# Kernel optimization log

Hardware: AMD Instinct MI355X
Metric: run time of the kernel (lower is better)

Reference implementation:

```python
import jax, jax.numpy as jnp
import numpy as np

N, E, B = 50000, 100000, 512   # nodes, edges, graphs
H, F_NODE, F_EDGE, T_OUT = 64, 16, 8, 1
T = 3                           # message-passing steps


def setup_inputs() -> dict:
    key = jax.random.key(0)
    ks = jax.random.split(key, 18)

    def w(k, shape, fan_in):
        return jax.random.normal(k, shape, dtype=jnp.float32) / np.sqrt(fan_in)

    return {
        "node_features": jax.random.normal(ks[0], (N, F_NODE), dtype=jnp.float32),
        "edge_features": jax.random.normal(ks[1], (E, F_EDGE), dtype=jnp.float32),
        "Esrc": jax.random.randint(ks[2], (E,), 0, N, dtype=jnp.int32),
        "Etgt": jax.random.randint(ks[3], (E,), 0, N, dtype=jnp.int32),
        "batch": jnp.sort(jax.random.randint(ks[4], (N,), 0, B, dtype=jnp.int32)),
        # input linear: node_features -> hidden
        "Win": w(ks[5], (H, F_NODE), F_NODE),
        "bin_": jnp.zeros((H,), jnp.float32),
        # edge encoder MLP: edge_features -> hidden -> hidden*hidden
        "We1": w(ks[6], (H, F_EDGE), F_EDGE),
        "be1": jnp.zeros((H,), jnp.float32),
        "We2": w(ks[7], (H * H, H), H),
        "be2": jnp.zeros((H * H,), jnp.float32),
        # GRU cell (shared across T steps)
        "Wih": w(ks[8], (3 * H, H), H),
        "bih": jnp.zeros((3 * H,), jnp.float32),
        "Whh": w(ks[9], (3 * H, H), H),
        "bhh": jnp.zeros((3 * H,), jnp.float32),
        # output linear: hidden -> target_features
        "Wout": w(ks[10], (T_OUT, H), H),
        "bout": jnp.zeros((T_OUT,), jnp.float32),
    }


def _gru(x, h, Wih, bih, Whh, bhh):
    gi = x @ Wih.T + bih            # [N, 3H]
    gh = h @ Whh.T + bhh
    i_r, i_z, i_n = jnp.split(gi, 3, axis=-1)
    h_r, h_z, h_n = jnp.split(gh, 3, axis=-1)
    r = jax.nn.sigmoid(i_r + h_r)
    z = jax.nn.sigmoid(i_z + h_z)
    n = jnp.tanh(i_n + r * h_n)
    return (1.0 - z) * n + z * h


def reference(node_features, edge_features, Esrc, Etgt, batch,
              Win, bin_, We1, be1, We2, be2,
              Wih, bih, Whh, bhh, Wout, bout):
    # Edge encoder MLP -> per-edge [H, H] message matrix (ENN style)
    eh = jax.nn.relu(edge_features @ We1.T + be1)          # [E, H]
    edge_data = (eh @ We2.T + be2).reshape(E, H, H)        # [E, H, H]

    x = node_features @ Win.T + bin_                       # [N, H]

    for _ in range(T):  # small fixed layer count
        msg = jnp.einsum('eij,ej->ei', edge_data, x[Esrc])  # per-edge matvec
        agg = jax.ops.segment_sum(msg, Etgt, num_segments=N)
        x = _gru(agg, x, Wih, bih, Whh, bhh)

    out = x @ Wout.T + bout                                # [N, 1]
    pooled = jax.ops.segment_sum(out, batch, num_segments=B)  # [B, 1]
    return pooled
```

## Files before the change

### kernel.cpp

```cpp
#include <hip/hip_runtime.h>
#include <hip/hip_fp16.h>

#define NN 50000
#define NE 100000
#define NB 512

typedef _Float16 f16x8 __attribute__((ext_vector_type(8)));
typedef _Float16 f16x4 __attribute__((ext_vector_type(4)));
typedef float f32x4  __attribute__((ext_vector_type(4)));
typedef float f32x16 __attribute__((ext_vector_type(16)));

__device__ __forceinline__ float sigm(float v) { return 1.0f / (1.0f + __expf(-v)); }
__device__ __forceinline__ float tanh_fast(float v) {
    float e = __expf(-2.0f * fabsf(v));
    float t = (1.0f - e) / (1.0f + e);
    return v < 0.f ? -t : t;
}

__global__ void fill0_kernel(float4* __restrict__ p, int n4)
{
    int i = blockIdx.x * 256 + threadIdx.x;
    const int stride = gridDim.x * 256;
    for (; i < n4; i += stride) p[i] = make_float4(0.f, 0.f, 0.f, 0.f);
}

__global__ __launch_bounds__(256) void node_in_kernel(
    const float* __restrict__ nf, const float* __restrict__ Win,
    const float* __restrict__ bin_, float* __restrict__ x, __half* __restrict__ xh)
{
    int idx = blockIdx.x * 256 + threadIdx.x;
    if (idx >= NN * 64) return;
    int n = idx >> 6, h = idx & 63;
    float acc = bin_[h];
    #pragma unroll
    for (int f = 0; f < 16; f++) acc += nf[n * 16 + f] * Win[h * 16 + f];
    x[idx] = acc;
    xh[idx] = __float2half(acc);
}

__global__ __launch_bounds__(256) void edge_l1_kernel(
    const float* __restrict__ ef, const float* __restrict__ We1,
    const float* __restrict__ be1, __half* __restrict__ ehh)
{
    int idx = blockIdx.x * 256 + threadIdx.x;
    if (idx >= NE * 64) return;
    int e = idx >> 6, k = idx & 63;
    float acc = be1[k];
    #pragma unroll
    for (int f = 0; f < 8; f++) acc += ef[e * 8 + f] * We1[k * 8 + f];
    ehh[idx] = __float2half(fmaxf(acc, 0.0f));
}

__global__ __launch_bounds__(256) void pack_b32_kernel(
    const float* __restrict__ We2, const float* __restrict__ be2,
    __half* __restrict__ Bp)
{
    int idx = blockIdx.x * 256 + threadIdx.x;
    if (idx >= 260 * 1024) return;
    int i  = idx & 7;
    int n  = (idx >> 3) & 31;
    int hi = (idx >> 8) & 1;
    int nt = (idx >> 9) & 1;
    int kt = idx >> 10;
    int p  = kt * 16 + hi * 8 + i;
    int col = nt * 32 + n;
    float v;
    if (p < 4096) {
        int j = p >> 6, k = p & 63;
        v = We2[((size_t)(col * 64 + j)) * 64 + k];
    } else {
        v = be2[col * 64 + (p - 4096)];
    }
    Bp[idx] = __float2half(v);
}

__global__ __launch_bounds__(256) void pack_gru_kernel(
    const float* __restrict__ Wih, const float* __restrict__ Whh,
    __half* __restrict__ WG)
{
    int idx = blockIdx.x * 256 + threadIdx.x;
    if (idx >= 24576) return;
    int kk = idx & 31;
    int n  = (idx >> 5) & 15;
    int nt = (idx >> 9) % 24;
    int kt = (idx >> 9) / 24;
    int k = kt * 32 + kk;
    int col192 = (nt % 12) * 16 + n;
    int gate = col192 >> 6, h = col192 & 63;
    const float* src = (nt < 12) ? Wih : Whh;
    WG[idx] = __float2half(src[((size_t)(gate * 64 + h)) * 64 + k]);
}

__global__ __launch_bounds__(128) void msg_kernel(
    const __half* __restrict__ xh, const __half* __restrict__ ehh,
    const __half* __restrict__ Bp,
    const int* __restrict__ Esrc, const int* __restrict__ Etgt,
    float* __restrict__ agg)
{
    __shared__ __attribute__((aligned(16))) __half xs[256 * 72];
    __shared__ __attribute__((aligned(16))) __half bst[16 * 1024];
    __shared__ int tgt_s[256];
    const int tid = threadIdx.x;
    const int e0 = blockIdx.x * 256;
    const int w = tid >> 6, lane = tid & 63;
    const int n32 = lane & 31, hi = lane >> 5;

    #pragma unroll
    for (int rr = 0; rr < 2; rr++) {
        const int row = rr * 128 + tid;
        const int e = e0 + row;
        const bool ok = (e < NE);
        const int src = ok ? Esrc[e] : 0;
        tgt_s[row] = ok ? Etgt[e] : -1;
        const uint4* xsrc = (const uint4*)(xh + (size_t)src * 64);
        #pragma unroll
        for (int i = 0; i < 8; i++) {
            uint4 v = ok ? xsrc[i] : make_uint4(0, 0, 0, 0);
            *(uint4*)(&xs[row * 72 + i * 8]) = v;
        }
    }

    __half2 ehc[4][4][4];
    #pragma unroll
    for (int mt = 0; mt < 4; mt++) {
        const int e = e0 + w * 128 + mt * 32 + n32;
        if (e < NE) {
            #pragma unroll
            for (int c4 = 0; c4 < 4; c4++) {
                union { uint4 u; __half2 h[4]; } u;
                u.u = *(const uint4*)(ehh + (size_t)e * 64 + c4 * 16 + hi * 8);
                #pragma unroll
                for (int q = 0; q < 4; q++) ehc[mt][c4][q] = u.h[q];
            }
        } else {
            __half2 z = __half2half2(__float2half(0.f));
            #pragma unroll
            for (int c4 = 0; c4 < 4; c4++)
                #pragma unroll
                for (int q = 0; q < 4; q++) ehc[mt][c4][q] = z;
        }
    }

    f32x16 acc[4][2];
    #pragma unroll
    for (int a = 0; a < 4; a++)
        #pragma unroll
        for (int b = 0; b < 2; b++)
            #pragma unroll
            for (int q = 0; q < 16; q++) acc[a][b][q] = 0.f;

    const __half* blane = bst + hi * 256 + n32 * 8;
    const int rbase = w * 128;

    #pragma unroll 1
    for (int c = 0; c < 17; c++) {
        const int niter = (c < 16) ? 16 : 4;
        __syncthreads();
        {
            const __half* gsrc = Bp + (size_t)c * 16384;
            for (int i = 0; i < niter; i++)
                *(uint4*)(bst + (size_t)(i * 128 + tid) * 8) =
                    *(const uint4*)(gsrc + (size_t)(i * 128 + tid) * 8);
        }
        __syncthreads();

        if (c < 16) {
            f16x4 xr4[4];
            #pragma unroll
            for (int mt = 0; mt < 4; mt++)
                xr4[mt] = *(const f16x4*)(xs + (rbase + mt * 32 + n32) * 72 + c * 4);
            #pragma unroll
            for (int u = 0; u < 16; u++) {
                f16x8 b0 = *(const f16x8*)(blane + u * 1024);
                f16x8 b1 = *(const f16x8*)(blane + u * 1024 + 512);
                const int c4 = u & 3;
                const int jq = u >> 2;
                #pragma unroll
                for (int mt = 0; mt < 4; mt++) {
                    union { f16x4 v; __half h[4]; } xu; xu.v = xr4[mt];
                    __half2 xv2 = __half2half2(xu.h[jq]);
                    union { __half2 h[4]; f16x8 v; } a;
                    #pragma unroll
                    for (int q = 0; q < 4; q++) a.h[q] = __hmul2(xv2, ehc[mt][c4][q]);
                    acc[mt][0] = __builtin_amdgcn_mfma_f32_32x32x16_f16(a.v, b0, acc[mt][0], 0, 0, 0);
                    acc[mt][1] = __builtin_amdgcn_mfma_f32_32x32x16_f16(a.v, b1, acc[mt][1], 0, 0, 0);
                }
            }
        } else {
            #pragma unroll
            for (int u = 0; u < 4; u++) {
                f16x8 b0 = *(const f16x8*)(blane + u * 1024);
                f16x8 b1 = *(const f16x8*)(blane + u * 1024 + 512);
                #pragma unroll
                for (int mt = 0; mt < 4; mt++) {
                    f16x8 a = *(const f16x8*)(xs + (rbase + mt * 32 + n32) * 72 + u * 16 + hi * 8);
                    acc[mt][0] = __builtin_amdgcn_mfma_f32_32x32x16_f16(a, b0, acc[mt][0], 0, 0, 0);
                    acc[mt][1] = __builtin_amdgcn_mfma_f32_32x32x16_f16(a, b1, acc[mt][1], 0, 0, 0);
                }
            }
        }
    }

    #pragma unroll
    for (int mt = 0; mt < 4; mt++) {
        #pragma unroll
        for (int r = 0; r < 16; r++) {
            const int rowe = (r & 3) + 8 * (r >> 2) + 4 * hi;
            const int t = tgt_s[rbase + mt * 32 + rowe];
            if (t >= 0) {
                atomicAdd(agg + (size_t)t * 64 + n32, acc[mt][0][r]);
                atomicAdd(agg + (size_t)t * 64 + 32 + n32, acc[mt][1][r]);
            }
        }
    }
}

__global__ __launch_bounds__(256, 2) void gru_kernel(
    const float* __restrict__ agg, float* __restrict__ x, __half* __restrict__ xh,
    const __half* __restrict__ WG,
    const float* __restrict__ bih, const float* __restrict__ bhh)
{
    __shared__ __attribute__((aligned(16))) __half wlds[24576];
    __shared__ __attribute__((aligned(16))) __half aggh[64 * 72];
    __shared__ __attribute__((aligned(16))) float xbuf[64 * 68];
    const int tid = threadIdx.x;
    const int node0 = blockIdx.x * 64;

    {
        const uint4* src = (const uint4*)WG;
        uint4* dst = (uint4*)wlds;
        #pragma unroll
        for (int i = 0; i < 12; i++) dst[i * 256 + tid] = src[i * 256 + tid];
    }
    #pragma unroll
    for (int i = 0; i < 4; i++) {
        int idx4 = i * 256 + tid;
        int nl = idx4 >> 4, c4 = idx4 & 15;
        int node = node0 + nl;
        float4 a = make_float4(0.f, 0.f, 0.f, 0.f);
        float4 xv = make_float4(0.f, 0.f, 0.f, 0.f);
        if (node < NN) {
            a  = *(const float4*)(agg + (size_t)node * 64 + c4 * 4);
            xv = *(const float4*)(x   + (size_t)node * 64 + c4 * 4);
        }
        __half2* ah = (__half2*)(aggh + nl * 72 + c4 * 4);
        ah[0] = __floats2half2_rn(a.x, a.y);
        ah[1] = __floats2half2_rn(a.z, a.w);
        *(float4*)(xbuf + nl * 68 + c4 * 4) = xv;
    }
    __syncthreads();

    const int w = tid >> 6, lane = tid & 63, m = lane & 15, quad = lane >> 4;
    const int nl_a = w * 16 + m;

    f16x8 a_agg[2], a_x[2];
    #pragma unroll
    for (int kt = 0; kt < 2; kt++) {
        const int koff = kt * 32 + quad * 8;
        a_agg[kt] = *(const f16x8*)(aggh + nl_a * 72 + koff);
        const float* xp = xbuf + nl_a * 68 + koff;
        union { __half2 h[4]; f16x8 v; } u;
        u.h[0] = __floats2half2_rn(xp[0], xp[1]);
        u.h[1] = __floats2half2_rn(xp[2], xp[3]);
        u.h[2] = __floats2half2_rn(xp[4], xp[5]);
        u.h[3] = __floats2half2_rn(xp[6], xp[7]);
        a_x[kt] = u.v;
    }

    f32x4 acc[24];
    #pragma unroll
    for (int nt = 0; nt < 24; nt++)
        #pragma unroll
        for (int q = 0; q < 4; q++) acc[nt][q] = 0.f;

    #pragma unroll
    for (int kt = 0; kt < 2; kt++) {
        #pragma unroll
        for (int nt = 0; nt < 24; nt++) {
            f16x8 b = *(const f16x8*)(wlds + (kt * 24 + nt) * 512 + m * 32 + quad * 8);
            acc[nt] = __builtin_amdgcn_mfma_f32_16x16x32_f16(
                (nt < 12) ? a_agg[kt] : a_x[kt], b, acc[nt], 0, 0, 0);
        }
    }

    #pragma unroll
    for (int t = 0; t < 4; t++) {
        const int h = t * 16 + m;
        const float bir = bih[h], biz = bih[64 + h], bin = bih[128 + h];
        const float bhr = bhh[h], bhz = bhh[64 + h], bhn = bhh[128 + h];
        #pragma unroll
        for (int r = 0; r < 4; r++) {
            const int nl = w * 16 + quad * 4 + r;
            float ir  = acc[t][r]      + bir;
            float iz  = acc[4 + t][r]  + biz;
            float in_ = acc[8 + t][r]  + bin;
            float hr  = acc[12 + t][r] + bhr;
            float hz  = acc[16 + t][r] + bhz;
            float hn  = acc[20 + t][r] + bhn;
            float rg = sigm(ir + hr);
            float z  = sigm(iz + hz);
            float n  = tanh_fast(in_ + rg * hn);
            float xold = xbuf[nl * 68 + h];
            xbuf[nl * 68 + h] = (1.0f - z) * n + z * xold;
        }
    }
    __syncthreads();

    #pragma unroll
    for (int i = 0; i < 4; i++) {
        int idx4 = i * 256 + tid;
        int nl = idx4 >> 4, c4 = idx4 & 15;
        int node = node0 + nl;
        if (node < NN) {
            float4 v = *(const float4*)(xbuf + nl * 68 + c4 * 4);
            *(float4*)(x + (size_t)node * 64 + c4 * 4) = v;
        }
    }
    #pragma unroll
    for (int i = 0; i < 2; i++) {
        int idx8 = i * 256 + tid;
        int nl = idx8 >> 3, c8 = idx8 & 7;
        int node = node0 + nl;
        if (node < NN) {
            const float* xp = xbuf + nl * 68 + c8 * 8;
            union { __half2 h[4]; uint4 u; } u;
            u.h[0] = __floats2half2_rn(xp[0], xp[1]);
            u.h[1] = __floats2half2_rn(xp[2], xp[3]);
            u.h[2] = __floats2half2_rn(xp[4], xp[5]);
            u.h[3] = __floats2half2_rn(xp[6], xp[7]);
            *(uint4*)(xh + (size_t)node * 64 + c8 * 8) = u.u;
        }
    }
}

__global__ __launch_bounds__(256) void pool_kernel(
    const float* __restrict__ x, const float* __restrict__ Wout,
    const float* __restrict__ bout, const int* __restrict__ batch,
    float* __restrict__ out)
{
    const int node = blockIdx.x * 256 + threadIdx.x;
    if (node >= NN) return;
    float acc = bout[0];
    const float4* xp = (const float4*)(x + (size_t)node * 64);
    #pragma unroll
    for (int i = 0; i < 16; i++) {
        float4 v = xp[i];
        acc += v.x * Wout[4*i] + v.y * Wout[4*i+1] + v.z * Wout[4*i+2] + v.w * Wout[4*i+3];
    }
    atomicAdd(out + batch[node], acc);
}

extern "C" void kernel_launch(void* const* d_in, const int* in_sizes, int n_in,
                              void* d_out, int out_size, void* d_ws, size_t ws_size,
                              hipStream_t stream)
{
    const float* nf   = (const float*)d_in[0];
    const float* ef   = (const float*)d_in[1];
    const int*   Esrc = (const int*)  d_in[2];
    const int*   Etgt = (const int*)  d_in[3];
    const int*   bat  = (const int*)  d_in[4];
    const float* Win  = (const float*)d_in[5];
    const float* bin_ = (const float*)d_in[6];
    const float* We1  = (const float*)d_in[7];
    const float* be1  = (const float*)d_in[8];
    const float* We2  = (const float*)d_in[9];
    const float* be2  = (const float*)d_in[10];
    const float* Wih  = (const float*)d_in[11];
    const float* bih  = (const float*)d_in[12];
    const float* Whh  = (const float*)d_in[13];
    const float* bhh  = (const float*)d_in[14];
    const float* Wout = (const float*)d_in[15];
    const float* bout = (const float*)d_in[16];

    char* ws = (char*)d_ws;
    float*  x   = (float*)(ws);
    float*  agg = (float*)(ws + 12800000);
    __half* xh  = (__half*)(ws + 25600000);
    __half* ehh = (__half*)(ws + 32000000);
    __half* Bp  = (__half*)(ws + 44800000);
    __half* WG  = (__half*)(ws + 45400064);

    hipMemsetAsync(d_out, 0, NB * sizeof(float), stream);

    node_in_kernel<<<(NN * 64 + 255) / 256, 256, 0, stream>>>(nf, Win, bin_, x, xh);
    edge_l1_kernel<<<(NE * 64 + 255) / 256, 256, 0, stream>>>(ef, We1, be1, ehh);
    pack_b32_kernel<<<(260 * 1024 + 255) / 256, 256, 0, stream>>>(We2, be2, Bp);
    pack_gru_kernel<<<(24576 + 255) / 256, 256, 0, stream>>>(Wih, Whh, WG);

    for (int t = 0; t < 3; t++) {
        fill0_kernel<<<1024, 256, 0, stream>>>((float4*)agg, NN * 16);
        msg_kernel<<<(NE + 255) / 256, 128, 0, stream>>>(xh, ehh, Bp, Esrc, Etgt, agg);
        gru_kernel<<<(NN + 63) / 64, 256, 0, stream>>>(agg, x, xh, WG, bih, bhh);
    }

    pool_kernel<<<(NN + 255) / 256, 256, 0, stream>>>(x, Wout, bout, bat, (float*)d_out);
}
```

Measured before the change: 486.7 us.

## Split msg kernel over K halves, drop fp32 state, fuse final GRU with pooling

The message kernel now launches two blocks per 256-edge tile, each covering half of the j-range, and reads B fragments straight from global/L2 instead of staging them through LDS with per-chunk barriers. The fp32 node state is removed, so the GRU reads and writes only the fp16 copy. The GRU kernel now zeroes agg itself, replacing the separate fill kernels. The last GRU step is fused with the output projection and per-graph pooling. This cuts launches, memory traffic and LDS synchronisation, but doubles the atomic adds into agg and keeps the hidden state in fp16 between steps, which may reduce accuracy.

```diff
diff --git a/kernel.cpp b/kernel.cpp
--- a/kernel.cpp
+++ b/kernel.cpp
@@ -26,7 +26,7 @@
 
 __global__ __launch_bounds__(256) void node_in_kernel(
     const float* __restrict__ nf, const float* __restrict__ Win,
-    const float* __restrict__ bin_, float* __restrict__ x, __half* __restrict__ xh)
+    const float* __restrict__ bin_, __half* __restrict__ xh)
 {
     int idx = blockIdx.x * 256 + threadIdx.x;
     if (idx >= NN * 64) return;
@@ -34,7 +34,6 @@
     float acc = bin_[h];
     #pragma unroll
     for (int f = 0; f < 16; f++) acc += nf[n * 16 + f] * Win[h * 16 + f];
-    x[idx] = acc;
     xh[idx] = __float2half(acc);
 }
 
@@ -91,17 +90,17 @@
     WG[idx] = __float2half(src[((size_t)(gate * 64 + h)) * 64 + k]);
 }
 
-__global__ __launch_bounds__(128) void msg_kernel(
+__global__ __launch_bounds__(128, 2) void msg_kernel(
     const __half* __restrict__ xh, const __half* __restrict__ ehh,
     const __half* __restrict__ Bp,
     const int* __restrict__ Esrc, const int* __restrict__ Etgt,
     float* __restrict__ agg)
 {
     __shared__ __attribute__((aligned(16))) __half xs[256 * 72];
-    __shared__ __attribute__((aligned(16))) __half bst[16 * 1024];
     __shared__ int tgt_s[256];
     const int tid = threadIdx.x;
-    const int e0 = blockIdx.x * 256;
+    const int eblk = blockIdx.x >> 1, ksel = blockIdx.x & 1;
+    const int e0 = eblk * 256;
     const int w = tid >> 6, lane = tid & 63;
     const int n32 = lane & 31, hi = lane >> 5;
 
@@ -140,6 +139,7 @@
                 for (int q = 0; q < 4; q++) ehc[mt][c4][q] = z;
         }
     }
+    __syncthreads();
 
     f32x16 acc[4][2];
     #pragma unroll
@@ -149,54 +149,47 @@
             #pragma unroll
             for (int q = 0; q < 16; q++) acc[a][b][q] = 0.f;
 
-    const __half* blane = bst + hi * 256 + n32 * 8;
     const int rbase = w * 128;
+    const __half* bbase = Bp + (size_t)ksel * 131072 + hi * 256 + n32 * 8;
 
     #pragma unroll 1
-    for (int c = 0; c < 17; c++) {
-        const int niter = (c < 16) ? 16 : 4;
-        __syncthreads();
-        {
-            const __half* gsrc = Bp + (size_t)c * 16384;
-            for (int i = 0; i < niter; i++)
-                *(uint4*)(bst + (size_t)(i * 128 + tid) * 8) =
-                    *(const uint4*)(gsrc + (size_t)(i * 128 + tid) * 8);
-        }
-        __syncthreads();
-
-        if (c < 16) {
-            f16x4 xr4[4];
+    for (int g = 0; g < 8; g++) {
+        const int jb = ksel * 32 + g * 4;
+        f16x4 xr4[4];
+        #pragma unroll
+        for (int mt = 0; mt < 4; mt++)
+            xr4[mt] = *(const f16x4*)(xs + (rbase + mt * 32 + n32) * 72 + jb);
+        #pragma unroll
+        for (int u = 0; u < 16; u++) {
+            const __half* bp = bbase + (size_t)(g * 16 + u) * 1024;
+            f16x8 b0 = *(const f16x8*)(bp);
+            f16x8 b1 = *(const f16x8*)(bp + 512);
+            const int c4 = u & 3;
+            const int jq = u >> 2;
             #pragma unroll
-            for (int mt = 0; mt < 4; mt++)
-                xr4[mt] = *(const f16x4*)(xs + (rbase + mt * 32 + n32) * 72 + c * 4);
+            for (int mt = 0; mt < 4; mt++) {
+                union { f16x4 v; __half h[4]; } xu; xu.v = xr4[mt];
+                __half2 xv2 = __half2half2(xu.h[jq]);
+                union { __half2 h[4]; f16x8 v; } a;
+                #pragma unroll
+                for (int q = 0; q < 4; q++) a.h[q] = __hmul2(xv2, ehc[mt][c4][q]);
+                acc[mt][0] = __builtin_amdgcn_mfma_f32_32x32x16_f16(a.v, b0, acc[mt][0], 0, 0, 0);
+                acc[mt][1] = __builtin_amdgcn_mfma_f32_32x32x16_f16(a.v, b1, acc[mt][1], 0, 0, 0);
+            }
+        }
+    }
+
+    if (ksel) {
+        #pragma unroll
+        for (int u = 0; u < 4; u++) {
+            const __half* bp = Bp + (size_t)(256 + u) * 1024 + hi * 256 + n32 * 8;
+            f16x8 b0 = *(const f16x8*)(bp);
+            f16x8 b1 = *(const f16x8*)(bp + 512);
             #pragma unroll
-            for (int u = 0; u < 16; u++) {
-                f16x8 b0 = *(const f16x8*)(blane + u * 1024);
-                f16x8 b1 = *(const f16x8*)(blane + u * 1024 + 512);
-                const int c4 = u & 3;
-                const int jq = u >> 2;
-                #pragma unroll
-                for (int mt = 0; mt < 4; mt++) {
-                    union { f16x4 v; __half h[4]; } xu; xu.v = xr4[mt];
-                    __half2 xv2 = __half2half2(xu.h[jq]);
-                    union { __half2 h[4]; f16x8 v; } a;
-                    #pragma unroll
-                    for (int q = 0; q < 4; q++) a.h[q] = __hmul2(xv2, ehc[mt][c4][q]);
-                    acc[mt][0] = __builtin_amdgcn_mfma_f32_32x32x16_f16(a.v, b0, acc[mt][0], 0, 0, 0);
-                    acc[mt][1] = __builtin_amdgcn_mfma_f32_32x32x16_f16(a.v, b1, acc[mt][1], 0, 0, 0);
-                }
-            }
-        } else {
-            #pragma unroll
-            for (int u = 0; u < 4; u++) {
-                f16x8 b0 = *(const f16x8*)(blane + u * 1024);
-                f16x8 b1 = *(const f16x8*)(blane + u * 1024 + 512);
-                #pragma unroll
-                for (int mt = 0; mt < 4; mt++) {
-                    f16x8 a = *(const f16x8*)(xs + (rbase + mt * 32 + n32) * 72 + u * 16 + hi * 8);
-                    acc[mt][0] = __builtin_amdgcn_mfma_f32_32x32x16_f16(a, b0, acc[mt][0], 0, 0, 0);
-                    acc[mt][1] = __builtin_amdgcn_mfma_f32_32x32x16_f16(a, b1, acc[mt][1], 0, 0, 0);
-                }
+            for (int mt = 0; mt < 4; mt++) {
+                f16x8 a = *(const f16x8*)(xs + (rbase + mt * 32 + n32) * 72 + u * 16 + hi * 8);
+                acc[mt][0] = __builtin_amdgcn_mfma_f32_32x32x16_f16(a, b0, acc[mt][0], 0, 0, 0);
+                acc[mt][1] = __builtin_amdgcn_mfma_f32_32x32x16_f16(a, b1, acc[mt][1], 0, 0, 0);
             }
         }
     }
@@ -216,13 +209,13 @@
 }
 
 __global__ __launch_bounds__(256, 2) void gru_kernel(
-    const float* __restrict__ agg, float* __restrict__ x, __half* __restrict__ xh,
+    float* __restrict__ agg, __half* __restrict__ xh,
     const __half* __restrict__ WG,
     const float* __restrict__ bih, const float* __restrict__ bhh)
 {
     __shared__ __attribute__((aligned(16))) __half wlds[24576];
     __shared__ __attribute__((aligned(16))) __half aggh[64 * 72];
-    __shared__ __attribute__((aligned(16))) float xbuf[64 * 68];
+    __shared__ __attribute__((aligned(16))) __half xhs[64 * 72];
     const int tid = threadIdx.x;
     const int node0 = blockIdx.x * 64;
 
@@ -238,15 +231,19 @@
         int nl = idx4 >> 4, c4 = idx4 & 15;
         int node = node0 + nl;
         float4 a = make_float4(0.f, 0.f, 0.f, 0.f);
-        float4 xv = make_float4(0.f, 0.f, 0.f, 0.f);
-        if (node < NN) {
-            a  = *(const float4*)(agg + (size_t)node * 64 + c4 * 4);
-            xv = *(const float4*)(x   + (size_t)node * 64 + c4 * 4);
-        }
+        if (node < NN) a = *(const float4*)(agg + (size_t)node * 64 + c4 * 4);
         __half2* ah = (__half2*)(aggh + nl * 72 + c4 * 4);
         ah[0] = __floats2half2_rn(a.x, a.y);
         ah[1] = __floats2half2_rn(a.z, a.w);
-        *(float4*)(xbuf + nl * 68 + c4 * 4) = xv;
+    }
+    #pragma unroll
+    for (int i = 0; i < 2; i++) {
+        int idx8 = i * 256 + tid;
+        int nl = idx8 >> 3, c8 = idx8 & 7;
+        int node = node0 + nl;
+        uint4 v = make_uint4(0, 0, 0, 0);
+        if (node < NN) v = *(const uint4*)(xh + (size_t)node * 64 + c8 * 8);
+        *(uint4*)(&xhs[nl * 72 + c8 * 8]) = v;
     }
     __syncthreads();
 
@@ -258,13 +255,7 @@
     for (int kt = 0; kt < 2; kt++) {
         const int koff = kt * 32 + quad * 8;
         a_agg[kt] = *(const f16x8*)(aggh + nl_a * 72 + koff);
-        const float* xp = xbuf + nl_a * 68 + koff;
-        union { __half2 h[4]; f16x8 v; } u;
-        u.h[0] = __floats2half2_rn(xp[0], xp[1]);
-        u.h[1] = __floats2half2_rn(xp[2], xp[3]);
-        u.h[2] = __floats2half2_rn(xp[4], xp[5]);
-        u.h[3] = __floats2half2_rn(xp[6], xp[7]);
-        a_x[kt] = u.v;
+        a_x[kt]   = *(const f16x8*)(xhs  + nl_a * 72 + koff);
     }
 
     f32x4 acc[24];
@@ -300,54 +291,136 @@
             float rg = sigm(ir + hr);
             float z  = sigm(iz + hz);
             float n  = tanh_fast(in_ + rg * hn);
-            float xold = xbuf[nl * 68 + h];
-            xbuf[nl * 68 + h] = (1.0f - z) * n + z * xold;
+            float xold = __half2float(xhs[nl * 72 + h]);
+            xhs[nl * 72 + h] = __float2half((1.0f - z) * n + z * xold);
         }
     }
     __syncthreads();
 
+    #pragma unroll
+    for (int i = 0; i < 2; i++) {
+        int idx8 = i * 256 + tid;
+        int nl = idx8 >> 3, c8 = idx8 & 7;
+        int node = node0 + nl;
+        if (node < NN)
+            *(uint4*)(xh + (size_t)node * 64 + c8 * 8) = *(const uint4*)(&xhs[nl * 72 + c8 * 8]);
+    }
     #pragma unroll
     for (int i = 0; i < 4; i++) {
         int idx4 = i * 256 + tid;
         int nl = idx4 >> 4, c4 = idx4 & 15;
         int node = node0 + nl;
-        if (node < NN) {
-            float4 v = *(const float4*)(xbuf + nl * 68 + c4 * 4);
-            *(float4*)(x + (size_t)node * 64 + c4 * 4) = v;
-        }
+        if (node < NN)
+            *(float4*)(agg + (size_t)node * 64 + c4 * 4) = make_float4(0.f, 0.f, 0.f, 0.f);
+    }
+}
+
+__global__ __launch_bounds__(256, 2) void gru_pool_kernel(
+    const float* __restrict__ agg, const __half* __restrict__ xh,
+    const __half* __restrict__ WG,
+    const float* __restrict__ bih, const float* __restrict__ bhh,
+    const float* __restrict__ Wout, const float* __restrict__ bout,
+    const int* __restrict__ batch, float* __restrict__ out)
+{
+    __shared__ __attribute__((aligned(16))) __half wlds[24576];
+    __shared__ __attribute__((aligned(16))) __half aggh[64 * 72];
+    __shared__ __attribute__((aligned(16))) __half xhs[64 * 72];
+    const int tid = threadIdx.x;
+    const int node0 = blockIdx.x * 64;
+
+    {
+        const uint4* src = (const uint4*)WG;
+        uint4* dst = (uint4*)wlds;
+        #pragma unroll
+        for (int i = 0; i < 12; i++) dst[i * 256 + tid] = src[i * 256 + tid];
+    }
+    #pragma unroll
+    for (int i = 0; i < 4; i++) {
+        int idx4 = i * 256 + tid;
+        int nl = idx4 >> 4, c4 = idx4 & 15;
+        int node = node0 + nl;
+        float4 a = make_float4(0.f, 0.f, 0.f, 0.f);
+        if (node < NN) a = *(const float4*)(agg + (size_t)node * 64 + c4 * 4);
+        __half2* ah = (__half2*)(aggh + nl * 72 + c4 * 4);
+        ah[0] = __floats2half2_rn(a.x, a.y);
+        ah[1] = __floats2half2_rn(a.z, a.w);
     }
     #pragma unroll
     for (int i = 0; i < 2; i++) {
         int idx8 = i * 256 + tid;
         int nl = idx8 >> 3, c8 = idx8 & 7;
         int node = node0 + nl;
-        if (node < NN) {
-            const float* xp = xbuf + nl * 68 + c8 * 8;
-            union { __half2 h[4]; uint4 u; } u;
-            u.h[0] = __floats2half2_rn(xp[0], xp[1]);
-            u.h[1] = __floats2half2_rn(xp[2], xp[3]);
-            u.h[2] = __floats2half2_rn(xp[4], xp[5]);
-            u.h[3] = __floats2half2_rn(xp[6], xp[7]);
-            *(uint4*)(xh + (size_t)node * 64 + c8 * 8) = u.u;
-        }
-    }
-}
-
-__global__ __launch_bounds__(256) void pool_kernel(
-    const float* __restrict__ x, const float* __restrict__ Wout,
-    const float* __restrict__ bout, const int* __restrict__ batch,
-    float* __restrict__ out)
-{
-    const int node = blockIdx.x * 256 + threadIdx.x;
-    if (node >= NN) return;
-    float acc = bout[0];
-    const float4* xp = (const float4*)(x + (size_t)node * 64);
-    #pragma unroll
-    for (int i = 0; i < 16; i++) {
-        float4 v = xp[i];
-        acc += v.x * Wout[4*i] + v.y * Wout[4*i+1] + v.z * Wout[4*i+2] + v.w * Wout[4*i+3];
-    }
-    atomicAdd(out + batch[node], acc);
+        uint4 v = make_uint4(0, 0, 0, 0);
+        if (node < NN) v = *(const uint4*)(xh + (size_t)node * 64 + c8 * 8);
+        *(uint4*)(&xhs[nl * 72 + c8 * 8]) = v;
+    }
+    __syncthreads();
+
+    const int w = tid >> 6, lane = tid & 63, m = lane & 15, quad = lane >> 4;
+    const int nl_a = w * 16 + m;
+    const int nbase = node0 + w * 16;
+
+    f16x8 a_agg[2], a_x[2];
+    #pragma unroll
+    for (int kt = 0; kt < 2; kt++) {
+        const int koff = kt * 32 + quad * 8;
+        a_agg[kt] = *(const f16x8*)(aggh + nl_a * 72 + koff);
+        a_x[kt]   = *(const f16x8*)(xhs  + nl_a * 72 + koff);
+    }
+
+    f32x4 acc[24];
+    #pragma unroll
+    for (int nt = 0; nt < 24; nt++)
+        #pragma unroll
+        for (int q = 0; q < 4; q++) acc[nt][q] = 0.f;
+
+    #pragma unroll
+    for (int kt = 0; kt < 2; kt++) {
+        #pragma unroll
+        for (int nt = 0; nt < 24; nt++) {
+            f16x8 b = *(const f16x8*)(wlds + (kt * 24 + nt) * 512 + m * 32 + quad * 8);
+            acc[nt] = __builtin_amdgcn_mfma_f32_16x16x32_f16(
+                (nt < 12) ? a_agg[kt] : a_x[kt], b, acc[nt], 0, 0, 0);
+        }
+    }
+
+    float po[4] = {0.f, 0.f, 0.f, 0.f};
+    #pragma unroll
+    for (int t = 0; t < 4; t++) {
+        const int h = t * 16 + m;
+        const float bir = bih[h], biz = bih[64 + h], bin = bih[128 + h];
+        const float bhr = bhh[h], bhz = bhh[64 + h], bhn = bhh[128 + h];
+        const float wo = Wout[h];
+        #pragma unroll
+        for (int r = 0; r < 4; r++) {
+            const int nl = w * 16 + quad * 4 + r;
+            float ir  = acc[t][r]      + bir;
+            float iz  = acc[4 + t][r]  + biz;
+            float in_ = acc[8 + t][r]  + bin;
+            float hr  = acc[12 + t][r] + bhr;
+            float hz  = acc[16 + t][r] + bhz;
+            float hn  = acc[20 + t][r] + bhn;
+            float rg = sigm(ir + hr);
+            float z  = sigm(iz + hz);
+            float n  = tanh_fast(in_ + rg * hn);
+            float xold = __half2float(xhs[nl * 72 + h]);
+            float xn = (1.0f - z) * n + z * xold;
+            po[r] += xn * wo;
+        }
+    }
+    #pragma unroll
+    for (int off = 1; off < 16; off <<= 1) {
+        #pragma unroll
+        for (int r = 0; r < 4; r++) po[r] += __shfl_xor(po[r], off, 64);
+    }
+    if (m == 0) {
+        const float b0 = bout[0];
+        #pragma unroll
+        for (int r = 0; r < 4; r++) {
+            const int nd = nbase + quad * 4 + r;
+            if (nd < NN) atomicAdd(out + batch[nd], po[r] + b0);
+        }
+    }
 }
 
 extern "C" void kernel_launch(void* const* d_in, const int* in_sizes, int n_in,
@@ -373,25 +446,26 @@
     const float* bout = (const float*)d_in[16];
 
     char* ws = (char*)d_ws;
-    float*  x   = (float*)(ws);
-    float*  agg = (float*)(ws + 12800000);
-    __half* xh  = (__half*)(ws + 25600000);
-    __half* ehh = (__half*)(ws + 32000000);
-    __half* Bp  = (__half*)(ws + 44800000);
-    __half* WG  = (__half*)(ws + 45400064);
+    float*  agg = (float*)(ws);
+    __half* xh  = (__half*)(ws + 12800000);
+    __half* ehh = (__half*)(ws + 19200000);
+    __half* Bp  = (__half*)(ws + 32000000);
+    __half* WG  = (__half*)(ws + 32600064);
 
     hipMemsetAsync(d_out, 0, NB * sizeof(float), stream);
 
-    node_in_kernel<<<(NN * 64 + 255) / 256, 256, 0, stream>>>(nf, Win, bin_, x, xh);
+    fill0_kernel<<<1024, 256, 0, stream>>>((float4*)agg, NN * 16);
+    node_in_kernel<<<(NN * 64 + 255) / 256, 256, 0, stream>>>(nf, Win, bin_, xh);
     edge_l1_kernel<<<(NE * 64 + 255) / 256, 256, 0, stream>>>(ef, We1, be1, ehh);
     pack_b32_kernel<<<(260 * 1024 + 255) / 256, 256, 0, stream>>>(We2, be2, Bp);
     pack_gru_kernel<<<(24576 + 255) / 256, 256, 0, stream>>>(Wih, Whh, WG);
 
-    for (int t = 0; t < 3; t++) {
-        fill0_kernel<<<1024, 256, 0, stream>>>((float4*)agg, NN * 16);
-        msg_kernel<<<(NE + 255) / 256, 128, 0, stream>>>(xh, ehh, Bp, Esrc, Etgt, agg);
-        gru_kernel<<<(NN + 63) / 64, 256, 0, stream>>>(agg, x, xh, WG, bih, bhh);
-    }
-
-    pool_kernel<<<(NN + 255) / 256, 256, 0, stream>>>(x, Wout, bout, bat, (float*)d_out);
-}
+    const int msg_grid = 2 * ((NE + 255) / 256);
+    for (int t = 0; t < 2; t++) {
+        msg_kernel<<<msg_grid, 128, 0, stream>>>(xh, ehh, Bp, Esrc, Etgt, agg);
+        gru_kernel<<<(NN + 63) / 64, 256, 0, stream>>>(agg, xh, WG, bih, bhh);
+    }
+    msg_kernel<<<msg_grid, 128, 0, stream>>>(xh, ehh, Bp, Esrc, Etgt, agg);
+    gru_pool_kernel<<<(NN + 63) / 64, 256, 0, stream>>>(
+        agg, xh, WG, bih, bhh, Wout, bout, bat, (float*)d_out);
+}
```

New measurement: 522.4 us. 1.07x slower.
